# Optimization experiments

Measured on AMD Instinct MI355X. Metric: run time of the kernel, lower is better.

The kernel has to match this reference:

```python
import jax, jax.numpy as jnp
import numpy as np

B, S, DM, H, FF = 2, 4096, 768, 12, 3072
WIN = 64  # one-sided window: attention_window=128 -> 64 each side
HD = DM // H


def layer_norm(x, g, b, eps=1e-5):
    mu = jnp.mean(x, axis=-1, keepdims=True)
    var = jnp.mean((x - mu) ** 2, axis=-1, keepdims=True)
    return (x - mu) / jnp.sqrt(var + eps) * g + b


def sliding_window_attention(q, k, v, w):
    # q,k,v: [B,H,S,D]; banded attention, each token sees [i-w, i+w]
    Bq, Hq, Sq, D = q.shape
    nc = Sq // w
    qc = (q * (1.0 / np.sqrt(D))).reshape(Bq, Hq, nc, w, D)
    kp = jnp.pad(k, ((0, 0), (0, 0), (w, w), (0, 0)))
    vp = jnp.pad(v, ((0, 0), (0, 0), (w, w), (0, 0)))
    # overlapping key windows of length 3w per query chunk
    idx = jnp.arange(nc)[:, None] * w + jnp.arange(3 * w)[None, :]  # [nc,3w]
    kw = kp[:, :, idx]  # [B,H,nc,3w,D]
    vw = vp[:, :, idx]
    scores = jnp.einsum('bhcqd,bhckd->bhcqk', qc, kw)  # [B,H,nc,w,3w]
    i = jnp.arange(w)[:, None]
    j = jnp.arange(3 * w)[None, :]
    band = (j >= i) & (j <= i + 2 * w)  # |rel pos| <= w
    gpos = jnp.arange(nc)[:, None, None] * w - w + j[None, :, :]  # key global pos [nc,1,3w]
    valid = band[None, :, :] & (gpos >= 0) & (gpos < Sq)  # [nc,w,3w]
    scores = jnp.where(valid[None, None], scores, -jnp.inf)
    probs = jax.nn.softmax(scores, axis=-1)
    out = jnp.einsum('bhcqk,bhckd->bhcqd', probs, vw)
    return out.reshape(Bq, Hq, Sq, D)


def setup_inputs() -> dict:
    key = jax.random.key(0)
    ks = jax.random.split(key, 8)
    sd = 1.0 / np.sqrt(DM)
    return {
        'x': jax.random.normal(ks[0], (B, S, DM), jnp.float32),
        'Wq': jax.random.normal(ks[1], (DM, DM), jnp.float32) * sd,
        'bq': jnp.zeros((DM,), jnp.float32),
        'Wk': jax.random.normal(ks[2], (DM, DM), jnp.float32) * sd,
        'bk': jnp.zeros((DM,), jnp.float32),
        'Wv': jax.random.normal(ks[3], (DM, DM), jnp.float32) * sd,
        'bv': jnp.zeros((DM,), jnp.float32),
        'ln1_g': jnp.ones((DM,), jnp.float32),
        'ln1_b': jnp.zeros((DM,), jnp.float32),
        'W1': jax.random.normal(ks[4], (DM, FF), jnp.float32) * sd,
        'b1': jnp.zeros((FF,), jnp.float32),
        'W2': jax.random.normal(ks[5], (FF, DM), jnp.float32) * (1.0 / np.sqrt(FF)),
        'b2': jnp.zeros((DM,), jnp.float32),
        'ln2_g': jnp.ones((DM,), jnp.float32),
        'ln2_b': jnp.zeros((DM,), jnp.float32),
    }


def reference(x, Wq, bq, Wk, bk, Wv, bv, ln1_g, ln1_b, W1, b1, W2, b2, ln2_g, ln2_b):
    Bx, Sx, d = x.shape

    def split_heads(t):
        return t.reshape(Bx, Sx, H, HD).transpose(0, 2, 1, 3)

    q = split_heads(x @ Wq + bq)
    k = split_heads(x @ Wk + bk)
    v = split_heads(x @ Wv + bv)
    attn = sliding_window_attention(q, k, v, WIN)  # [B,H,S,D]
    attn = attn.transpose(0, 2, 1, 3).reshape(Bx, Sx, d)
    # Longformer self-attention here has no output projection; residual directly
    x1 = layer_norm(attn + x, ln1_g, ln1_b)
    ff = jax.nn.gelu(x1 @ W1 + b1) @ W2 + b2
    return layer_norm(ff + x1, ln2_g, ln2_b)
```

## Files before the change

### kernel.cpp

```cpp
#include <hip/hip_runtime.h>
#include <cstdint>
#include <cstddef>

#define S_LEN   4096
#define D_MODEL 768
#define N_HEADS 12
#define HEAD_DIM 64
#define FF_DIM  3072
#define B_SZ    2
#define M_ROWS  (B_SZ * S_LEN)
#define QKV_N   (3 * D_MODEL)

typedef unsigned short u16;
typedef __attribute__((ext_vector_type(8))) __bf16 bf16x8;
typedef __attribute__((ext_vector_type(4))) float  f32x4;

__device__ __forceinline__ float bf2f(u16 u) {
    union { unsigned u32; float f; } cv; cv.u32 = ((unsigned)u) << 16; return cv.f;
}
__device__ __forceinline__ u16 f2bf(float f) {
    __bf16 b = (__bf16)f;
    union { __bf16 b; u16 u; } cv; cv.b = b; return cv.u;
}
__device__ __forceinline__ float gelu_fast(float x) {
    float x2 = x * x;
    float u  = x * fmaf(0.035677408f, x2, 0.7978845608f);
    float e  = __expf(-2.f * u);
    return x * __builtin_amdgcn_rcpf(1.f + e);
}
__device__ __forceinline__ void async16(const void* g, void* l) {
    __builtin_amdgcn_global_load_lds(
        (const __attribute__((address_space(1))) unsigned int*)g,
        (__attribute__((address_space(3))) unsigned int*)l, 16, 0, 0);
}

__global__ __launch_bounds__(256) void cvt_x(const float* __restrict__ in,
                                             u16* __restrict__ out, long n8)
{
    long i = (long)blockIdx.x * 256 + threadIdx.x;
    const long stride = (long)gridDim.x * 256;
    for (; i < n8; i += stride) {
        const float* p = in + i * 8;
        float4 a = *(const float4*)p;
        float4 b = *(const float4*)(p + 4);
        union { uint4 q; u16 el[8]; } o;
        o.el[0] = f2bf(a.x); o.el[1] = f2bf(a.y);
        o.el[2] = f2bf(a.z); o.el[3] = f2bf(a.w);
        o.el[4] = f2bf(b.x); o.el[5] = f2bf(b.y);
        o.el[6] = f2bf(b.z); o.el[7] = f2bf(b.w);
        ((uint4*)out)[i] = o.q;
    }
}

__global__ __launch_bounds__(256) void transpose_w(const float* __restrict__ inA,
                                                   const float* __restrict__ inB,
                                                   const float* __restrict__ inC,
                                                   u16* __restrict__ out,
                                                   int R, int C)
{
    __shared__ __align__(16) u16 T[64 * 72];
    const int z = blockIdx.z;
    const float* in = (z == 0) ? inA : (z == 1) ? inB : inC;
    u16* o_ = out + (size_t)z * R * C;
    const int r0 = blockIdx.y * 64, c0 = blockIdx.x * 64;
    const int t = threadIdx.x;
    for (int v = t; v < 512; v += 256) {
        int rr = v >> 3, c8 = (v & 7) * 8;
        const float* p = in + (size_t)(r0 + rr) * C + c0 + c8;
        float4 a = *(const float4*)p;
        float4 b = *(const float4*)(p + 4);
        union { uint4 q; u16 el[8]; } o;
        o.el[0] = f2bf(a.x); o.el[1] = f2bf(a.y);
        o.el[2] = f2bf(a.z); o.el[3] = f2bf(a.w);
        o.el[4] = f2bf(b.x); o.el[5] = f2bf(b.y);
        o.el[6] = f2bf(b.z); o.el[7] = f2bf(b.w);
        *(uint4*)&T[rr * 72 + c8] = o.q;
    }
    __syncthreads();
    for (int v = t; v < 512; v += 256) {
        int cc = v >> 3, r8 = (v & 7) * 8;
        union { uint4 q; u16 el[8]; } tmp;
        #pragma unroll
        for (int e = 0; e < 8; ++e) tmp.el[e] = T[(r8 + e) * 72 + cc];
        *(uint4*)&o_[(size_t)(c0 + cc) * R + r0 + r8] = tmp.q;
    }
}

__global__ __launch_bounds__(256) void pack_qkv_bias(const float* bq, const float* bk,
                                                     const float* bv, float* biasqkv)
{
    int i = blockIdx.x * 256 + threadIdx.x;
    if (i < 768) {
        biasqkv[i]        = bq[i];
        biasqkv[768 + i]  = bk[i];
        biasqkv[1536 + i] = bv[i];
    }
}

template<int MI>
__global__ __launch_bounds__(256) void gemm_bt_t(const u16* __restrict__ A,
                                                 const u16* __restrict__ BT,
                                                 const float* __restrict__ bias,
                                                 void* __restrict__ C,
                                                 int M, int N, int K, int act, int ofp32)
{
    constexpr int TM = MI * 32;
    __shared__ __align__(16) u16 As[TM * 64];
    __shared__ __align__(16) u16 Bs[128 * 64];
    const int t = threadIdx.x;

    const int NX = gridDim.x, MY8 = gridDim.y >> 3;
    const int L = blockIdx.y * NX + blockIdx.x;
    const int xcd = L & 7, q = L >> 3;
    const long m0 = (long)(xcd * MY8 + q / NX) * TM;
    const long n0 = (long)(q % NX) * 128;

    const int lane = t & 63, w = t >> 6;
    const int wm = (w >> 1) * (MI * 16), wn = (w & 1) * 64;
    const int lr = lane & 15, lq = lane >> 4;

    const int r0 = t >> 3;
    const int cg = ((t & 7) ^ (r0 & 7)) * 8;
    const u16* pa = &A[(m0 + r0) * (long)K + cg];
    const u16* pb = &BT[(n0 + r0) * (long)K + cg];
    char* la = (char*)As + t * 16;
    char* lb = (char*)Bs + t * 16;

    f32x4 acc[MI][4] = {};

    for (int k0 = 0; k0 < K; k0 += 64) {
        #pragma unroll
        for (int p = 0; p < MI; ++p)
            async16(pa + k0 + p * 32 * (long)K, la + p * 4096);
        #pragma unroll
        for (int p = 0; p < 4; ++p)
            async16(pb + k0 + p * 32 * (long)K, lb + p * 4096);
        __syncthreads();
        #pragma unroll
        for (int ks = 0; ks < 2; ++ks) {
            const int kc = ((ks * 4 + lq) ^ (lr & 7)) * 8;
            bf16x8 af[MI], bfr[4];
            #pragma unroll
            for (int mi = 0; mi < MI; ++mi)
                af[mi] = *(const bf16x8*)&As[(wm + mi * 16 + lr) * 64 + kc];
            #pragma unroll
            for (int ni = 0; ni < 4; ++ni)
                bfr[ni] = *(const bf16x8*)&Bs[(wn + ni * 16 + lr) * 64 + kc];
            #pragma unroll
            for (int mi = 0; mi < MI; ++mi)
                #pragma unroll
                for (int ni = 0; ni < 4; ++ni)
                    acc[mi][ni] = __builtin_amdgcn_mfma_f32_16x16x32_bf16(
                        af[mi], bfr[ni], acc[mi][ni], 0, 0, 0);
        }
        __syncthreads();
    }

    #pragma unroll
    for (int mi = 0; mi < MI; ++mi) {
        #pragma unroll
        for (int ni = 0; ni < 4; ++ni) {
            const long colg = n0 + wn + ni * 16 + lr;
            const float bv = bias[colg];
            #pragma unroll
            for (int r = 0; r < 4; ++r) {
                const long row = m0 + wm + mi * 16 + lq * 4 + r;
                float v = acc[mi][ni][r] + bv;
                if (act == 1) v = gelu_fast(v);
                if (ofp32) ((float*)C)[row * (long)N + colg] = v;
                else       ((u16*)C)[row * (long)N + colg] = f2bf(v);
            }
        }
    }
}

__global__ __launch_bounds__(256) void attn_mfma(const u16* __restrict__ qkv,
                                                 u16* __restrict__ attn_out)
{
    const int c = blockIdx.x;
    const int h = blockIdx.y;
    const int b = blockIdx.z;
    const int t = threadIdx.x;
    const int wave = t >> 6, lane = t & 63;
    const int lr = lane & 15, lq = lane >> 4;

    __shared__ __align__(16) u16 Ps[64 * 200];
    __shared__ __align__(16) u16 VT[64 * 200];
    __shared__ float linv[64];

    const long base = (long)b * S_LEN;
    const long qrow0 = base + c * 64;

    for (int v = t; v < 1536; v += 256) {
        int j = v >> 3, d8 = (v & 7) * 8;
        int s = c * 64 - 64 + j;
        int scl = s < 0 ? 0 : (s > S_LEN - 1 ? S_LEN - 1 : s);
        uint4 raw = *(const uint4*)&qkv[(base + scl) * (long)QKV_N + 2 * D_MODEL + h * 64 + d8];
        union { uint4 q; u16 el[8]; } u; u.q = raw;
        #pragma unroll
        for (int e = 0; e < 8; ++e) VT[(d8 + e) * 200 + j] = u.el[e];
    }

    bf16x8 aq[2];
    #pragma unroll
    for (int ks = 0; ks < 2; ++ks)
        aq[ks] = *(const bf16x8*)&qkv[(qrow0 + wave * 16 + lr) * (long)QKV_N
                                      + h * 64 + ks * 32 + lq * 8];

    f32x4 sacc[12];
    #pragma unroll
    for (int nt = 0; nt < 12; ++nt) {
        int key = nt * 16 + lr;
        int s = c * 64 - 64 + key;
        int scl = s < 0 ? 0 : (s > S_LEN - 1 ? S_LEN - 1 : s);
        const u16* kp = &qkv[(base + scl) * (long)QKV_N + D_MODEL + h * 64 + lq * 8];
        bf16x8 bk0 = *(const bf16x8*)kp;
        bf16x8 bk1 = *(const bf16x8*)(kp + 32);
        f32x4 z = {0.f, 0.f, 0.f, 0.f};
        z = __builtin_amdgcn_mfma_f32_16x16x32_bf16(aq[0], bk0, z, 0, 0, 0);
        z = __builtin_amdgcn_mfma_f32_16x16x32_bf16(aq[1], bk1, z, 0, 0, 0);
        sacc[nt] = z;
    }

    float sc_[12][4];
    float m[4] = {-1e30f, -1e30f, -1e30f, -1e30f};
    #pragma unroll
    for (int nt = 0; nt < 12; ++nt) {
        const int j = nt * 16 + lr;
        const int gpos = c * 64 - 64 + j;
        #pragma unroll
        for (int r = 0; r < 4; ++r) {
            const int qi = wave * 16 + lq * 4 + r;
            const bool ok = (j >= qi) && (j <= qi + 128) && (gpos >= 0) && (gpos < S_LEN);
            const float v = ok ? sacc[nt][r] * 0.125f : -1e30f;
            sc_[nt][r] = v;
            m[r] = fmaxf(m[r], v);
        }
    }
    #pragma unroll
    for (int o = 1; o < 16; o <<= 1)
        #pragma unroll
        for (int r = 0; r < 4; ++r) m[r] = fmaxf(m[r], __shfl_xor(m[r], o));

    float sum[4] = {0.f, 0.f, 0.f, 0.f};
    #pragma unroll
    for (int nt = 0; nt < 12; ++nt)
        #pragma unroll
        for (int r = 0; r < 4; ++r) {
            const float e = __expf(sc_[nt][r] - m[r]);
            sc_[nt][r] = e;
            sum[r] += e;
        }
    #pragma unroll
    for (int o = 1; o < 16; o <<= 1)
        #pragma unroll
        for (int r = 0; r < 4; ++r) sum[r] += __shfl_xor(sum[r], o);

    #pragma unroll
    for (int nt = 0; nt < 12; ++nt)
        #pragma unroll
        for (int r = 0; r < 4; ++r)
            Ps[(wave * 16 + lq * 4 + r) * 200 + nt * 16 + lr] = f2bf(sc_[nt][r]);
    if (lr == 0) {
        #pragma unroll
        for (int r = 0; r < 4; ++r)
            linv[wave * 16 + lq * 4 + r] = 1.f / sum[r];
    }
    __syncthreads();

    f32x4 oacc[4] = {};
    #pragma unroll
    for (int ks = 0; ks < 6; ++ks) {
        bf16x8 ap = *(const bf16x8*)&Ps[(wave * 16 + lr) * 200 + ks * 32 + lq * 8];
        #pragma unroll
        for (int nt = 0; nt < 4; ++nt) {
            bf16x8 bv = *(const bf16x8*)&VT[(nt * 16 + lr) * 200 + ks * 32 + lq * 8];
            oacc[nt] = __builtin_amdgcn_mfma_f32_16x16x32_bf16(ap, bv, oacc[nt], 0, 0, 0);
        }
    }

    #pragma unroll
    for (int nt = 0; nt < 4; ++nt) {
        #pragma unroll
        for (int r = 0; r < 4; ++r) {
            const int row = wave * 16 + lq * 4 + r;
            const float o = oacc[nt][r] * linv[row];
            attn_out[(qrow0 + row) * (long)D_MODEL + h * 64 + nt * 16 + lr] = f2bf(o);
        }
    }
}

__global__ __launch_bounds__(256) void ln_kernel(const void* a, int af32,
                                                 const u16* b,
                                                 const float* __restrict__ g,
                                                 const float* __restrict__ beta,
                                                 void* out, int of32)
{
    const long r = blockIdx.x;
    const int t = threadIdx.x;
    float v[3];
    float s = 0.f, s2 = 0.f;
    #pragma unroll
    for (int ii = 0; ii < 3; ++ii) {
        const long j = ii * 256 + t;
        const long idx = r * D_MODEL + j;
        const float xa = af32 ? ((const float*)a)[idx] : bf2f(((const u16*)a)[idx]);
        const float x = xa + bf2f(b[idx]);
        v[ii] = x; s += x; s2 += x * x;
    }
    #pragma unroll
    for (int off = 32; off > 0; off >>= 1) {
        s  += __shfl_down(s, off);
        s2 += __shfl_down(s2, off);
    }
    __shared__ float rs_[4], rs2_[4];
    int w = t >> 6, lane = t & 63;
    if (lane == 0) { rs_[w] = s; rs2_[w] = s2; }
    __syncthreads();
    float S1 = rs_[0] + rs_[1] + rs_[2] + rs_[3];
    float S2 = rs2_[0] + rs2_[1] + rs2_[2] + rs2_[3];
    float mu   = S1 * (1.f / 768.f);
    float var  = S2 * (1.f / 768.f) - mu * mu;
    float rstd = rsqrtf(var + 1e-5f);
    #pragma unroll
    for (int ii = 0; ii < 3; ++ii) {
        const long j = ii * 256 + t;
        const float o = (v[ii] - mu) * rstd * g[j] + beta[j];
        if (of32) ((float*)out)[r * D_MODEL + j] = o;
        else      ((u16*)out)[r * D_MODEL + j] = f2bf(o);
    }
}

extern "C" void kernel_launch(void* const* d_in, const int* in_sizes, int n_in,
                              void* d_out, int out_size, void* d_ws, size_t ws_size,
                              hipStream_t stream)
{
    const float* x    = (const float*)d_in[0];
    const float* Wq   = (const float*)d_in[1];
    const float* bq   = (const float*)d_in[2];
    const float* Wk   = (const float*)d_in[3];
    const float* bk   = (const float*)d_in[4];
    const float* Wv   = (const float*)d_in[5];
    const float* bv   = (const float*)d_in[6];
    const float* ln1g = (const float*)d_in[7];
    const float* ln1b = (const float*)d_in[8];
    const float* W1   = (const float*)d_in[9];
    const float* b1   = (const float*)d_in[10];
    const float* W2   = (const float*)d_in[11];
    const float* b2   = (const float*)d_in[12];
    const float* ln2g = (const float*)d_in[13];
    const float* ln2b = (const float*)d_in[14];

    char* ws = (char*)d_ws;
    size_t off = 0;
    u16* WqkvT  = (u16*)(ws + off);   off += (size_t)QKV_N * D_MODEL * 2;
    u16* W1T    = (u16*)(ws + off);   off += (size_t)FF_DIM * D_MODEL * 2;
    u16* W2T    = (u16*)(ws + off);   off += (size_t)D_MODEL * FF_DIM * 2;
    float* biasqkv = (float*)(ws + off); off += (size_t)QKV_N * 4;
    u16* big    = (u16*)(ws + off);   off += (size_t)M_ROWS * FF_DIM * 2;
    u16* x1     = (u16*)(ws + off);   off += (size_t)M_ROWS * D_MODEL * 2;

    u16* xbf    = big;
    u16* qkv    = big + (size_t)M_ROWS * D_MODEL;
    u16* hbuf   = big;
    u16* attnb  = (u16*)d_out;
    float* outf = (float*)d_out;

    dim3 blk(256);
    cvt_x<<<dim3(1024), blk, 0, stream>>>(x, xbf, (long)M_ROWS * D_MODEL / 8);
    transpose_w<<<dim3(12, 12, 3), blk, 0, stream>>>(Wq, Wk, Wv, WqkvT, 768, 768);
    transpose_w<<<dim3(48, 12, 1), blk, 0, stream>>>(W1, W1, W1, W1T, 768, 3072);
    transpose_w<<<dim3(12, 48, 1), blk, 0, stream>>>(W2, W2, W2, W2T, 3072, 768);
    pack_qkv_bias<<<dim3(3), blk, 0, stream>>>(bq, bk, bv, biasqkv);

    gemm_bt_t<4><<<dim3(QKV_N / 128, M_ROWS / 128), blk, 0, stream>>>(
        xbf, WqkvT, biasqkv, qkv, M_ROWS, QKV_N, D_MODEL, 0, 0);
    attn_mfma<<<dim3(64, N_HEADS, B_SZ), blk, 0, stream>>>(qkv, attnb);
    ln_kernel<<<dim3(M_ROWS), blk, 0, stream>>>(attnb, 0, xbf, ln1g, ln1b, x1, 0);
    gemm_bt_t<4><<<dim3(FF_DIM / 128, M_ROWS / 128), blk, 0, stream>>>(
        x1, W1T, b1, hbuf, M_ROWS, FF_DIM, D_MODEL, 1, 0);
    gemm_bt_t<2><<<dim3(D_MODEL / 128, M_ROWS / 64), blk, 0, stream>>>(
        hbuf, W2T, b2, outf, M_ROWS, D_MODEL, FF_DIM, 0, 1);
    ln_kernel<<<dim3(M_ROWS), blk, 0, stream>>>(outf, 1, x1, ln2g, ln2b, outf, 1);
}
```

Before: 339.2 us.

## Add 256x256-tile 8-wave GEMM with XCD-aware block mapping for QKV and FF1

```diff
diff --git a/kernel.cpp b/kernel.cpp
--- a/kernel.cpp
+++ b/kernel.cpp
@@ -174,6 +174,146 @@
     }
 }
 
+__device__ __forceinline__ void stage4(const u16* p, long K, long kk, char* dst) {
+    #pragma unroll
+    for (int hh = 0; hh < 4; ++hh)
+        async16(p + (long)hh * 64 * K + kk, dst + hh * 8192);
+}
+
+__global__ __launch_bounds__(512) void gemm256(const u16* __restrict__ A,
+                                               const u16* __restrict__ BT,
+                                               const float* __restrict__ bias,
+                                               void* __restrict__ C,
+                                               int M, int N, int K, int act, int ofp32)
+{
+    __shared__ __align__(16) u16 As[2][256 * 64];
+    __shared__ __align__(16) u16 Bs[2][256 * 64];
+    const int t = threadIdx.x;
+
+    const int NX = gridDim.x, MY8 = gridDim.y >> 3;
+    const int L = blockIdx.y * NX + blockIdx.x;
+    const int xcd = L & 7, q = L >> 3;
+    const long m0 = (long)(xcd * MY8 + q / NX) * 256;
+    const long n0 = (long)(q % NX) * 256;
+
+    const int lane = t & 63, w = t >> 6;
+    const int wm = w >> 2, wn = w & 3;
+    const int lr = lane & 15, lq = lane >> 4;
+
+    const int r0 = t >> 3;
+    const int cg = ((t & 7) ^ (r0 & 7)) * 8;
+    const u16* pa = &A[(m0 + r0) * (long)K + cg];
+    const u16* pb = &BT[(n0 + r0) * (long)K + cg];
+    char* laA = (char*)&As[0][0] + t * 16;
+    char* laB = (char*)&Bs[0][0] + t * 16;
+
+    const int kc0 = ((0 + lq) ^ (lr & 7)) * 8;
+    const int kc1 = ((4 + lq) ^ (lr & 7)) * 8;
+    const int rowA = wm * 128 + lr;
+    const int rowB = wn * 64 + lr;
+
+    f32x4 acc[8][4] = {};
+    const int NT = K >> 6;
+
+    stage4(pa, K, 0, laA);
+    stage4(pb, K, 0, laB);
+
+    for (int kt = 0; kt < NT; ++kt) {
+        const int cb = kt & 1;
+        const u16* Asb = As[cb];
+        const u16* Bsb = Bs[cb];
+        bf16x8 af[4], bf0[4];
+
+        if (kt + 1 < NT) {
+            stage4(pa, K, (long)(kt + 1) * 64, laA + (cb ^ 1) * 32768);
+            asm volatile("s_waitcnt vmcnt(4)" ::: "memory");
+        } else {
+            asm volatile("s_waitcnt vmcnt(0)" ::: "memory");
+        }
+        __builtin_amdgcn_s_barrier();
+        asm volatile("" ::: "memory");
+        #pragma unroll
+        for (int ni = 0; ni < 4; ++ni)
+            bf0[ni] = *(const bf16x8*)&Bsb[(rowB + ni * 16) * 64 + kc0];
+        #pragma unroll
+        for (int mi = 0; mi < 4; ++mi)
+            af[mi] = *(const bf16x8*)&Asb[(rowA + mi * 16) * 64 + kc0];
+        __builtin_amdgcn_s_setprio(1);
+        #pragma unroll
+        for (int mi = 0; mi < 4; ++mi)
+            #pragma unroll
+            for (int ni = 0; ni < 4; ++ni)
+                acc[mi][ni] = __builtin_amdgcn_mfma_f32_16x16x32_bf16(
+                    af[mi], bf0[ni], acc[mi][ni], 0, 0, 0);
+        __builtin_amdgcn_s_setprio(0);
+        __builtin_amdgcn_s_barrier();
+
+        #pragma unroll
+        for (int mi = 0; mi < 4; ++mi)
+            af[mi] = *(const bf16x8*)&Asb[(rowA + 64 + mi * 16) * 64 + kc0];
+        if (kt + 1 < NT)
+            stage4(pb, K, (long)(kt + 1) * 64, laB + (cb ^ 1) * 32768);
+        __builtin_amdgcn_s_barrier();
+        __builtin_amdgcn_s_setprio(1);
+        #pragma unroll
+        for (int mi = 0; mi < 4; ++mi)
+            #pragma unroll
+            for (int ni = 0; ni < 4; ++ni)
+                acc[4 + mi][ni] = __builtin_amdgcn_mfma_f32_16x16x32_bf16(
+                    af[mi], bf0[ni], acc[4 + mi][ni], 0, 0, 0);
+        __builtin_amdgcn_s_setprio(0);
+        __builtin_amdgcn_s_barrier();
+
+        #pragma unroll
+        for (int ni = 0; ni < 4; ++ni)
+            bf0[ni] = *(const bf16x8*)&Bsb[(rowB + ni * 16) * 64 + kc1];
+        #pragma unroll
+        for (int mi = 0; mi < 4; ++mi)
+            af[mi] = *(const bf16x8*)&Asb[(rowA + mi * 16) * 64 + kc1];
+        __builtin_amdgcn_s_barrier();
+        __builtin_amdgcn_s_setprio(1);
+        #pragma unroll
+        for (int mi = 0; mi < 4; ++mi)
+            #pragma unroll
+            for (int ni = 0; ni < 4; ++ni)
+                acc[mi][ni] = __builtin_amdgcn_mfma_f32_16x16x32_bf16(
+                    af[mi], bf0[ni], acc[mi][ni], 0, 0, 0);
+        __builtin_amdgcn_s_setprio(0);
+        __builtin_amdgcn_s_barrier();
+
+        #pragma unroll
+        for (int mi = 0; mi < 4; ++mi)
+            af[mi] = *(const bf16x8*)&Asb[(rowA + 64 + mi * 16) * 64 + kc1];
+        __builtin_amdgcn_s_barrier();
+        __builtin_amdgcn_s_setprio(1);
+        #pragma unroll
+        for (int mi = 0; mi < 4; ++mi)
+            #pragma unroll
+            for (int ni = 0; ni < 4; ++ni)
+                acc[4 + mi][ni] = __builtin_amdgcn_mfma_f32_16x16x32_bf16(
+                    af[mi], bf0[ni], acc[4 + mi][ni], 0, 0, 0);
+        __builtin_amdgcn_s_setprio(0);
+        __builtin_amdgcn_s_barrier();
+    }
+
+    #pragma unroll
+    for (int mi = 0; mi < 8; ++mi) {
+        #pragma unroll
+        for (int ni = 0; ni < 4; ++ni) {
+            const long colg = n0 + wn * 64 + ni * 16 + lr;
+            const float bv = bias[colg];
+            #pragma unroll
+            for (int r = 0; r < 4; ++r) {
+                const long row = m0 + wm * 128 + mi * 16 + lq * 4 + r;
+                float v = acc[mi][ni][r] + bv;
+                if (act == 1) v = gelu_fast(v);
+                if (ofp32) ((float*)C)[row * (long)N + colg] = v;
+                else       ((u16*)C)[row * (long)N + colg]  = f2bf(v);
+            }
+        }
+    }
+}
+
 __global__ __launch_bounds__(256) void attn_mfma(const u16* __restrict__ qkv,
                                                  u16* __restrict__ attn_out)
 {
@@ -373,11 +513,11 @@
     transpose_w<<<dim3(12, 48, 1), blk, 0, stream>>>(W2, W2, W2, W2T, 3072, 768);
     pack_qkv_bias<<<dim3(3), blk, 0, stream>>>(bq, bk, bv, biasqkv);
 
-    gemm_bt_t<4><<<dim3(QKV_N / 128, M_ROWS / 128), blk, 0, stream>>>(
+    gemm256<<<dim3(QKV_N / 256, M_ROWS / 256), dim3(512), 0, stream>>>(
         xbf, WqkvT, biasqkv, qkv, M_ROWS, QKV_N, D_MODEL, 0, 0);
     attn_mfma<<<dim3(64, N_HEADS, B_SZ), blk, 0, stream>>>(qkv, attnb);
     ln_kernel<<<dim3(M_ROWS), blk, 0, stream>>>(attnb, 0, xbf, ln1g, ln1b, x1, 0);
-    gemm_bt_t<4><<<dim3(FF_DIM / 128, M_ROWS / 128), blk, 0, stream>>>(
+    gemm256<<<dim3(FF_DIM / 256, M_ROWS / 256), dim3(512), 0, stream>>>(
         x1, W1T, b1, hbuf, M_ROWS, FF_DIM, D_MODEL, 1, 0);
     gemm_bt_t<2><<<dim3(D_MODEL / 128, M_ROWS / 64), blk, 0, stream>>>(
         hbuf, W2T, b2, outf, M_ROWS, D_MODEL, FF_DIM, 0, 1);
```

New measurement: 375.1 us. +10.6%, slower.
